# Kernel optimization log

Hardware: AMD Instinct MI355X
Metric: run time of the kernel (lower is better)

Reference implementation:

```python
import jax, jax.numpy as jnp
import numpy as np

H, HP, NH_M, NH_D = 1024, 64, 8, 8
B, T = 2, 2048
SPARSITY = 8
N_ROT = 32  # int(0.5 * HP), even
BASE = 10000.0


def _rope(x, pos, n_rot, base):
    # x: (..., L, d); pos: broadcastable to (..., L). Rotates first n_rot dims.
    half = n_rot // 2
    inv = base ** (-jnp.arange(half, dtype=x.dtype) / half)  # (half,)
    ang = pos[..., None] * inv                               # (..., L, half)
    cos, sin = jnp.cos(ang), jnp.sin(ang)
    x1, x2 = x[..., :half], x[..., half:n_rot]
    rot = jnp.concatenate([x1 * cos - x2 * sin, x1 * sin + x2 * cos], axis=-1)
    return jnp.concatenate([rot, x[..., n_rot:]], axis=-1)


def setup_inputs() -> dict:
    key = jax.random.key(0)
    ks = jax.random.split(key, 6)
    s = 0.02
    return {
        "X": jax.random.normal(ks[0], (B, T, H), jnp.float32),
        "mosa_router_w": jax.random.normal(ks[1], (H, NH_M), jnp.float32) * s,
        "mosa_wqkv": jax.random.normal(ks[2], (H, NH_M, 3 * HP), jnp.float32) * s,
        "mosa_wo": jax.random.normal(ks[3], (NH_M * HP, H), jnp.float32) * s,
        "dense_wqkv": jax.random.normal(ks[4], (H, NH_D, 3 * HP), jnp.float32) * s,
        "dense_wo": jax.random.normal(ks[5], (NH_D * HP, H), jnp.float32) * s,
    }


def _mosa_branch(X, router_w, wqkv, wo):
    # Expert-choice sparse attention: each head routes its own top-k tokens.
    b, t, _ = X.shape
    k = t // SPARSITY
    scores = jnp.einsum('bth,hn->bnt', X, router_w)                      # (b,nh,T)
    _, idx = jax.lax.top_k(scores, k)                                    # (b,nh,k)
    idx = jnp.sort(idx, axis=-1)                                         # keep temporal order
    gates = jax.nn.sigmoid(jnp.take_along_axis(scores, idx, axis=-1))    # (b,nh,k)
    Xg = jnp.take_along_axis(X[:, None], idx[..., None], axis=2)         # (b,nh,k,h)
    qkv = jnp.einsum('bnkh,hnd->bnkd', Xg, wqkv)                         # (b,nh,k,3hp)
    Q, K, V = jnp.split(qkv, 3, axis=-1)
    pos = idx.astype(X.dtype)                                            # original positions for RoPE
    Q = _rope(Q, pos, N_ROT, BASE)
    K = _rope(K, pos, N_ROT, BASE)
    att = jnp.einsum('bnqd,bnkd->bnqk', Q, K) / jnp.sqrt(jnp.asarray(HP, X.dtype))
    causal = idx[..., :, None] >= idx[..., None, :]                      # causality by original index
    att = jnp.where(causal, att, -jnp.inf)
    AV = jnp.einsum('bnqk,bnkd->bnqd', jax.nn.softmax(att, axis=-1), V)
    AV = AV * gates[..., None]
    # scatter selected-token outputs back to full sequence
    out = jnp.zeros((b, NH_M, t, HP), X.dtype)
    bi = jnp.arange(b)[:, None, None]
    hi = jnp.arange(NH_M)[None, :, None]
    out = out.at[bi, hi, idx].set(AV)                                    # (b,nh,T,hp)
    out = out.transpose(0, 2, 1, 3).reshape(b, t, NH_M * HP)
    return out @ wo


def _dense_branch(X, wqkv, wo):
    b, t, _ = X.shape
    qkv = jnp.einsum('bth,hnd->bntd', X, wqkv)                           # (b,nh,T,3hp)
    Q, K, V = jnp.split(qkv, 3, axis=-1)
    pos = jnp.arange(t, dtype=X.dtype)
    Q = _rope(Q, pos, N_ROT, BASE)
    K = _rope(K, pos, N_ROT, BASE)
    att = jnp.einsum('bnqd,bnkd->bnqk', Q, K) / jnp.sqrt(jnp.asarray(HP, X.dtype))
    causal = jnp.tril(jnp.ones((t, t), bool))
    att = jnp.where(causal, att, -jnp.inf)
    AV = jnp.einsum('bnqk,bnkd->bnqd', jax.nn.softmax(att, axis=-1), V)  # (b,nh,T,hp)
    return AV.transpose(0, 2, 1, 3).reshape(b, t, NH_D * HP) @ wo


def reference(X, mosa_router_w, mosa_wqkv, mosa_wo, dense_wqkv, dense_wo):
    return (_mosa_branch(X, mosa_router_w, mosa_wqkv, mosa_wo)
            + _dense_branch(X, dense_wqkv, dense_wo))
```

## Files before the change

kernel.cpp:

```cpp
#include <hip/hip_runtime.h>
#include <math.h>

constexpr int BB = 2;
constexpr int SEQ = 2048;
constexpr int HD = 1024;
constexpr int DH = 64;
constexpr int NHEAD = 8;
constexpr int D3 = 192;
constexpr int KSEL = 256;
constexpr float NEG = -1e30f;

typedef short short8 __attribute__((ext_vector_type(8)));
typedef float f32x4 __attribute__((ext_vector_type(4)));

__device__ __forceinline__ ushort bf16u(float f) {
  union { float f; unsigned u; } v; v.f = f;
  unsigned r = (v.u + 0x7FFFu + ((v.u >> 16) & 1u)) >> 16;
  return (ushort)r;
}
__device__ __forceinline__ float bf2f(ushort h) {
  union { unsigned u; float f; } v; v.u = ((unsigned)h) << 16;
  return v.f;
}

__device__ __forceinline__ unsigned long long rankkey(float s, int idx) {
  union { float f; unsigned u; } v; v.f = s;
  unsigned o = (v.u & 0x80000000u) ? ~v.u : (v.u | 0x80000000u);
  return ((unsigned long long)o << 11) | (unsigned)(2047 - idx);
}

__global__ void cast_bf16x4(const float* __restrict__ x, ushort* __restrict__ y, int n4) {
  int i = blockIdx.x * 256 + threadIdx.x;
  if (i >= n4) return;
  float4 v = ((const float4*)x)[i];
  ushort4 r; r.x = bf16u(v.x); r.y = bf16u(v.y); r.z = bf16u(v.z); r.w = bf16u(v.w);
  ((ushort4*)y)[i] = r;
}

__global__ __launch_bounds__(256) void transpose_cast2(
    const float* __restrict__ W1, ushort* __restrict__ T1,
    const float* __restrict__ W2, ushort* __restrict__ T2, int K, int N) {
  const float* W = blockIdx.z ? W2 : W1;
  ushort* Wt = blockIdx.z ? T2 : T1;
  __shared__ float tile[32][33];
  int n0 = blockIdx.x * 32, k0 = blockIdx.y * 32;
  int tx = threadIdx.x & 31, ty = threadIdx.x >> 5;
#pragma unroll
  for (int i = 0; i < 4; i++)
    tile[ty + 8 * i][tx] = W[(size_t)(k0 + ty + 8 * i) * N + n0 + tx];
  __syncthreads();
#pragma unroll
  for (int i = 0; i < 4; i++)
    Wt[(size_t)(n0 + ty + 8 * i) * K + k0 + tx] = bf16u(tile[tx][ty + 8 * i]);
}

__global__ __launch_bounds__(256) void router2(const float* __restrict__ X,
    const float* __restrict__ rw, float* __restrict__ scores) {
  __shared__ float rwT[8][8][132];
  int tid = threadIdx.x;
  for (int idx = tid; idx < 8192; idx += 256) {
    int h = idx & 1023, n = idx >> 10;
    rwT[n][h >> 7][h & 127] = rw[h * 8 + n];
  }
  __syncthreads();
  int row = blockIdx.x * 32 + (tid >> 3);
  int seg = tid & 7;
  const float* xrow = X + (size_t)row * HD + seg * 128;
  float acc[8] = {};
#pragma unroll 8
  for (int it = 0; it < 32; it++) {
    float4 xv = *(const float4*)(xrow + 4 * it);
#pragma unroll
    for (int n = 0; n < 8; n++) {
      float4 rv = *(const float4*)&rwT[n][seg][4 * it];
      acc[n] += xv.x * rv.x + xv.y * rv.y + xv.z * rv.z + xv.w * rv.w;
    }
  }
#pragma unroll
  for (int n = 0; n < 8; n++) {
    acc[n] += __shfl_xor(acc[n], 1);
    acc[n] += __shfl_xor(acc[n], 2);
    acc[n] += __shfl_xor(acc[n], 4);
  }
  int b = row >> 11, t2 = row & (SEQ - 1);
  scores[((size_t)b * NHEAD + seg) * SEQ + t2] = acc[seg];
}

__global__ __launch_bounds__(256) void topk_partial(const float* __restrict__ scores,
    int* __restrict__ pranks) {
  int row = blockIdx.x;
  int c = blockIdx.y;
  __shared__ unsigned long long ck[64];
  const float* sp = scores + (size_t)row * SEQ;
  int tid = threadIdx.x;
  if (tid < 64) ck[tid] = rankkey(sp[c * 64 + tid], c * 64 + tid);
  __syncthreads();
  unsigned long long kv[8]; int p[8];
#pragma unroll
  for (int i = 0; i < 8; i++) {
    int vi = i * 256 + tid;
    kv[i] = rankkey(sp[vi], vi);
    p[i] = 0;
  }
#pragma unroll 8
  for (int j = 0; j < 64; j += 2) {
    unsigned long long k0 = ck[j], k1 = ck[j + 1];
#pragma unroll
    for (int i = 0; i < 8; i++) {
      p[i] += (k0 > kv[i]);
      p[i] += (k1 > kv[i]);
    }
  }
#pragma unroll
  for (int i = 0; i < 8; i++)
    pranks[((size_t)row * 32 + c) * SEQ + i * 256 + tid] = p[i];
}

__global__ __launch_bounds__(1024) void topk_select(const float* __restrict__ scores,
    const int* __restrict__ pranks, int* __restrict__ sel, float* __restrict__ gates) {
  int bn = blockIdx.x;
  __shared__ int wsum[16];
  int tid = threadIdx.x;
  int t0 = tid * 2;
  int r0 = 0, r1 = 0;
#pragma unroll
  for (int c = 0; c < 32; c++) {
    const int2 pp = *(const int2*)&pranks[((size_t)bn * 32 + c) * SEQ + t0];
    r0 += pp.x; r1 += pp.y;
  }
  int f0 = r0 < KSEL, f1 = r1 < KSEL;
  unsigned long long b0 = __ballot(f0), b1 = __ballot(f1);
  int lane = tid & 63, wv = tid >> 6;
  unsigned long long lower = (1ULL << lane) - 1ULL;
  int before = __popcll(b0 & lower) + __popcll(b1 & lower);
  int wtotal = __popcll(b0) + __popcll(b1);
  if (lane == 0) wsum[wv] = wtotal;
  __syncthreads();
  int woff = 0;
#pragma unroll
  for (int i2 = 0; i2 < 16; i2++) woff += (i2 < wv) ? wsum[i2] : 0;
  int base = woff + before;
  if (f0) { sel[bn * KSEL + base] = t0;
            gates[bn * KSEL + base] = 1.f / (1.f + __expf(-scores[(size_t)bn * SEQ + t0]));
            base++; }
  if (f1) { sel[bn * KSEL + base] = t0 + 1;
            gates[bn * KSEL + base] = 1.f / (1.f + __expf(-scores[(size_t)bn * SEQ + t0 + 1])); }
}

__global__ __launch_bounds__(256) void gemm_mosa_bf16(const ushort* __restrict__ Xb,
    const ushort* __restrict__ Wt, const int* __restrict__ sel,
    ushort* __restrict__ Qmg, ushort* __restrict__ Kmg, ushort* __restrict__ Vtmg) {
  __shared__ __align__(16) ushort As[64][40];
  __shared__ __align__(16) ushort Bs[64][40];
  int bn = blockIdx.x; int b = bn >> 3, n = bn & 7;
  int m0 = blockIdx.y * 64, n0 = blockIdx.z * 64;
  int tid = threadIdx.x;
  int lane = tid & 63, w = tid >> 6;
  int wm = w & 1, wn = w >> 1;
  int cc = lane & 15, quad = lane >> 4;
  int sr = tid >> 2, sc4 = tid & 3;

  int grow = sel[bn * KSEL + m0 + sr];
  const ushort* arow = Xb + ((size_t)(b * SEQ) + grow) * HD;
  const ushort* brow = Wt + ((size_t)(n * D3 + n0 + sr)) * HD;

  f32x4 acc[2][2];
#pragma unroll
  for (int i = 0; i < 2; i++)
#pragma unroll
    for (int j = 0; j < 2; j++)
#pragma unroll
      for (int r = 0; r < 4; r++) acc[i][j][r] = 0.f;

  for (int k0 = 0; k0 < HD; k0 += 32) {
    __syncthreads();
    *(short8*)&As[sr][8 * sc4] = *(const short8*)(arow + k0 + 8 * sc4);
    *(short8*)&Bs[sr][8 * sc4] = *(const short8*)(brow + k0 + 8 * sc4);
    __syncthreads();
    short8 af[2], bf_[2];
#pragma unroll
    for (int i = 0; i < 2; i++) af[i] = *(const short8*)&As[32 * wm + 16 * i + cc][8 * quad];
#pragma unroll
    for (int j = 0; j < 2; j++) bf_[j] = *(const short8*)&Bs[32 * wn + 16 * j + cc][8 * quad];
#pragma unroll
    for (int i = 0; i < 2; i++)
#pragma unroll
      for (int j = 0; j < 2; j++)
        acc[i][j] = __builtin_amdgcn_mfma_f32_16x16x32_bf16(af[i], bf_[j], acc[i][j], 0, 0, 0);
  }

#pragma unroll
  for (int i = 0; i < 2; i++)
#pragma unroll
    for (int j = 0; j < 2; j++) {
      int col = n0 + 32 * wn + 16 * j + cc;
      int row0 = m0 + 32 * wm + 16 * i + 4 * quad;
      if (col < 64) {
#pragma unroll
        for (int r = 0; r < 4; r++)
          Qmg[((size_t)bn * KSEL + row0 + r) * 64 + col] = bf16u(acc[i][j][r] * 0.125f);
      } else if (col < 128) {
#pragma unroll
        for (int r = 0; r < 4; r++)
          Kmg[((size_t)bn * KSEL + row0 + r) * 64 + (col - 64)] = bf16u(acc[i][j][r]);
      } else {
        ushort4 pk;
        pk.x = bf16u(acc[i][j][0]); pk.y = bf16u(acc[i][j][1]);
        pk.z = bf16u(acc[i][j][2]); pk.w = bf16u(acc[i][j][3]);
        *(ushort4*)&Vtmg[((size_t)bn * 64 + (col - 128)) * KSEL + row0] = pk;
      }
    }
}

__global__ void rope_split(ushort* __restrict__ Qb, ushort* __restrict__ Kb,
                           const int* __restrict__ sel, int mosa) {
  int tid = blockIdx.x * 256 + threadIdx.x;
  int j = tid & 15;
  int which = (tid >> 4) & 1;
  int row = tid >> 5;
  float pos = mosa ? (float)sel[row] : (float)(row & (SEQ - 1));
  float inv = __expf((float)j * -0.5756462732485115f);
  float ang = pos * inv;
  float c = cosf(ang), sn = sinf(ang);
  ushort* p = (which ? Kb : Qb) + (size_t)row * 64 + j;
  float x1 = bf2f(p[0]), x2 = bf2f(p[16]);
  p[0] = bf16u(x1 * c - x2 * sn);
  p[16] = bf16u(x1 * sn + x2 * c);
}

template <bool MOSA>
__global__ __launch_bounds__(512) void flash4(
    const ushort* __restrict__ Qg, const ushort* __restrict__ Kg,
    const ushort* __restrict__ Vtg, const int* __restrict__ sel,
    const float* __restrict__ gates, ushort* __restrict__ outp, int nqt) {
  __shared__ __align__(16) ushort Qs[2][64][64];
  __shared__ __align__(16) ushort Ks[64][64];
  __shared__ __align__(16) ushort Vt[64][64];
  __shared__ __align__(16) ushort Ps[2][64][64];

  const int T = MOSA ? KSEL : SEQ;
  int bn = blockIdx.y; int b = bn >> 3, n = bn & 7;
  int pair = blockIdx.x;
  int qtA = pair, qtB = nqt - 1 - pair;
  int tid = threadIdx.x;
  int g = tid >> 8;
  int myqt = g ? qtB : qtA;
  int t = tid & 255;
  int lane = tid & 63, w = (tid >> 6) & 3;
  int cc = lane & 15, quad = lane >> 4;

  const ushort* Qb = Qg + (size_t)bn * T * 64;
  const ushort* Kb = Kg + (size_t)bn * T * 64;
  const ushort* Vb = Vtg + (size_t)bn * 64 * T;

  {
    int r = t >> 2, c = t & 3;
    const ushort* src = Qb + (size_t)(myqt * 64 + r) * 64;
    *(short8*)&Qs[g][r][8 * (c ^ (r & 7))] = *(const short8*)(src + 8 * c);
    int c2 = c + 4;
    *(short8*)&Qs[g][r][8 * (c2 ^ (r & 7))] = *(const short8*)(src + 8 * c2);
  }

  f32x4 oacc[4];
  float m = NEG, l = 0.f;
#pragma unroll
  for (int jd = 0; jd < 4; jd++)
#pragma unroll
    for (int r = 0; r < 4; r++) oacc[jd][r] = 0.f;

  for (int kt = 0; kt <= qtB; kt++) {
    __syncthreads();
    {
      int r = tid >> 3, c = tid & 7;
      *(short8*)&Ks[r][8 * (c ^ (r & 7))] =
          *(const short8*)(Kb + (size_t)(kt * 64 + r) * 64 + 8 * c);
      *(short8*)&Vt[r][8 * (c ^ (r & 7))] =
          *(const short8*)(Vb + (size_t)r * T + kt * 64 + 8 * c);
    }
    __syncthreads();

    if (g || (kt <= qtA)) {
      f32x4 sacc[4];
#pragma unroll
      for (int j = 0; j < 4; j++)
#pragma unroll
        for (int r = 0; r < 4; r++) sacc[j][r] = 0.f;
      int qrow = 16 * w + cc;
#pragma unroll
      for (int ks = 0; ks < 2; ks++) {
        short8 bq = *(const short8*)&Qs[g][qrow][8 * ((quad + 4 * ks) ^ (qrow & 7))];
#pragma unroll
        for (int j = 0; j < 4; j++) {
          int krow = 16 * j + cc;
          short8 ak = *(const short8*)&Ks[krow][8 * ((quad + 4 * ks) ^ (krow & 7))];
          sacc[j] = __builtin_amdgcn_mfma_f32_16x16x32_bf16(ak, bq, sacc[j], 0, 0, 0);
        }
      }
      if (kt == myqt) {
#pragma unroll
        for (int j = 0; j < 4; j++)
#pragma unroll
          for (int r = 0; r < 4; r++)
            if (16 * j + 4 * quad + r > 16 * w + cc) sacc[j][r] = NEG;
      }
      float mx = NEG;
#pragma unroll
      for (int j = 0; j < 4; j++)
#pragma unroll
        for (int r = 0; r < 4; r++) mx = fmaxf(mx, sacc[j][r]);
      mx = fmaxf(mx, __shfl_xor(mx, 16));
      mx = fmaxf(mx, __shfl_xor(mx, 32));
      float mn = fmaxf(m, mx);
      float sc = __expf(m - mn);
      m = mn;
      float rsum = 0.f;
      float p[4][4];
#pragma unroll
      for (int j = 0; j < 4; j++)
#pragma unroll
        for (int r = 0; r < 4; r++) { p[j][r] = __expf(sacc[j][r] - mn); rsum += p[j][r]; }
      rsum += __shfl_xor(rsum, 16);
      rsum += __shfl_xor(rsum, 32);
      l = l * sc + rsum;
#pragma unroll
      for (int j = 0; j < 4; j++) {
        ushort4 pk;
        pk.x = bf16u(p[j][0]); pk.y = bf16u(p[j][1]);
        pk.z = bf16u(p[j][2]); pk.w = bf16u(p[j][3]);
        int phys = (2 * j + (quad >> 1)) ^ (qrow & 7);
        *(ushort4*)&Ps[g][qrow][phys * 8 + 4 * (quad & 1)] = pk;
      }
#pragma unroll
      for (int r = 0; r < 4; r++) {
        float scr = __shfl(sc, 16 * quad + 4 * quad + r);
#pragma unroll
        for (int jd = 0; jd < 4; jd++) oacc[jd][r] *= scr;
      }
      __asm__ volatile("s_waitcnt lgkmcnt(0)" ::: "memory");
#pragma unroll
      for (int ks = 0; ks < 2; ks++) {
        short8 ap = *(const short8*)&Ps[g][qrow][8 * ((quad + 4 * ks) ^ (qrow & 7))];
#pragma unroll
        for (int jd = 0; jd < 4; jd++) {
          int vrow = 16 * jd + cc;
          short8 bv = *(const short8*)&Vt[vrow][8 * ((quad + 4 * ks) ^ (vrow & 7))];
          oacc[jd] = __builtin_amdgcn_mfma_f32_16x16x32_bf16(ap, bv, oacc[jd], 0, 0, 0);
        }
      }
    }
  }

#pragma unroll
  for (int r = 0; r < 4; r++) {
    float lr = __shfl(l, 16 * quad + 4 * quad + r);
    int q = myqt * 64 + 16 * w + 4 * quad + r;
    float scale;
    size_t row;
    if (MOSA) {
      int trow = sel[bn * KSEL + q];
      scale = gates[bn * KSEL + q] / lr;
      row = (size_t)(b * SEQ + trow);
    } else {
      scale = 1.f / lr;
      row = (size_t)(b * SEQ + q);
    }
    ushort* orow = outp + row * (NHEAD * DH) + n * DH;
#pragma unroll
    for (int jd = 0; jd < 4; jd++)
      orow[16 * jd + cc] = bf16u(oacc[jd][r] * scale);
  }
}

template <int MODE>
__global__ __launch_bounds__(256) void gemm_bf16(
    const ushort* __restrict__ A1, const ushort* __restrict__ B1t, int K1,
    const ushort* __restrict__ A2, const ushort* __restrict__ B2t, int K2,
    void* __restrict__ outv, int N,
    ushort* __restrict__ Qo, ushort* __restrict__ Ko, ushort* __restrict__ Vto) {
  __shared__ __align__(16) ushort As[128][32];
  __shared__ __align__(16) ushort Bs[128][32];
  int m0 = blockIdx.x * 128, n0 = blockIdx.y * 128;
  int tid = threadIdx.x;
  int lane = tid & 63, wave = tid >> 6;
  int wm = wave & 1, wn = wave >> 1;
  int cc = lane & 15, quad = lane >> 4;
  int sr = tid >> 2, sc = tid & 3;

  f32x4 acc[4][4];
#pragma unroll
  for (int i = 0; i < 4; i++)
#pragma unroll
    for (int j = 0; j < 4; j++)
#pragma unroll
      for (int r = 0; r < 4; r++) acc[i][j][r] = 0.f;

  const int npass = (MODE == 0) ? 2 : 1;
  for (int pass = 0; pass < npass; pass++) {
    const ushort* A = pass ? A2 : A1;
    const ushort* Bt = pass ? B2t : B1t;
    int K = pass ? K2 : K1;
    for (int k0 = 0; k0 < K; k0 += 32) {
      __syncthreads();
      {
        short8 a0 = *(const short8*)(A + (size_t)(m0 + sr) * K + k0 + 8 * sc);
        short8 a1 = *(const short8*)(A + (size_t)(m0 + sr + 64) * K + k0 + 8 * sc);
        short8 b0 = *(const short8*)(Bt + (size_t)(n0 + sr) * K + k0 + 8 * sc);
        short8 b1 = *(const short8*)(Bt + (size_t)(n0 + sr + 64) * K + k0 + 8 * sc);
        *(short8*)&As[sr][8 * ((sc + (sr >> 1)) & 3)] = a0;
        *(short8*)&As[sr + 64][8 * ((sc + ((sr + 64) >> 1)) & 3)] = a1;
        *(short8*)&Bs[sr][8 * ((sc + (sr >> 1)) & 3)] = b0;
        *(short8*)&Bs[sr + 64][8 * ((sc + ((sr + 64) >> 1)) & 3)] = b1;
      }
      __syncthreads();
      short8 af[4], bfr[4];
#pragma unroll
      for (int i = 0; i < 4; i++) {
        int ra = 64 * wm + 16 * i + cc;
        af[i] = *(const short8*)&As[ra][8 * ((quad + (ra >> 1)) & 3)];
      }
#pragma unroll
      for (int j = 0; j < 4; j++) {
        int rb = 64 * wn + 16 * j + cc;
        bfr[j] = *(const short8*)&Bs[rb][8 * ((quad + (rb >> 1)) & 3)];
      }
#pragma unroll
      for (int i = 0; i < 4; i++)
#pragma unroll
        for (int j = 0; j < 4; j++)
          acc[i][j] = __builtin_amdgcn_mfma_f32_16x16x32_bf16(af[i], bfr[j], acc[i][j], 0, 0, 0);
    }
  }

#pragma unroll
  for (int i = 0; i < 4; i++) {
#pragma unroll
    for (int j = 0; j < 4; j++) {
      int colg = n0 + 64 * wn + 16 * j + cc;
      int row0 = m0 + 64 * wm + 16 * i + 4 * quad;
      if (MODE == 0) {
#pragma unroll
        for (int r = 0; r < 4; r++)
          ((float*)outv)[(size_t)(row0 + r) * N + colg] = acc[i][j][r];
      } else {
        int nn = colg / 192, c = colg % 192;
        int b2 = row0 >> 11, t2 = row0 & 2047;
        int bn2 = b2 * 8 + nn;
        if (c < 64) {
#pragma unroll
          for (int r = 0; r < 4; r++)
            Qo[((size_t)bn2 * SEQ + t2 + r) * 64 + c] = bf16u(acc[i][j][r] * 0.125f);
        } else if (c < 128) {
#pragma unroll
          for (int r = 0; r < 4; r++)
            Ko[((size_t)bn2 * SEQ + t2 + r) * 64 + (c - 64)] = bf16u(acc[i][j][r]);
        } else {
          ushort4 pk;
          pk.x = bf16u(acc[i][j][0]); pk.y = bf16u(acc[i][j][1]);
          pk.z = bf16u(acc[i][j][2]); pk.w = bf16u(acc[i][j][3]);
          *(ushort4*)&Vto[((size_t)bn2 * 64 + (c - 128)) * SEQ + t2] = pk;
        }
      }
    }
  }
}

extern "C" void kernel_launch(void* const* d_in, const int* in_sizes, int n_in,
                              void* d_out, int out_size, void* d_ws, size_t ws_size,
                              hipStream_t stream) {
  const float* X          = (const float*)d_in[0];
  const float* router_w   = (const float*)d_in[1];
  const float* mosa_wqkv  = (const float*)d_in[2];
  const float* mosa_wo    = (const float*)d_in[3];
  const float* dense_wqkv = (const float*)d_in[4];
  const float* dense_wo   = (const float*)d_in[5];
  float* out = (float*)d_out;
  char* ws = (char*)d_ws;

  float*  scores  = (float*) (ws + 0);
  int*    sel     = (int*)   (ws + 131072);
  float*  gates   = (float*) (ws + 147456);
  ushort* avm     = (ushort*)(ws + 163840);
  ushort* avd     = (ushort*)(ws + 4358144);
  ushort* Xb      = (ushort*)(ws + 8552448);
  ushort* Wqkv_t  = (ushort*)(ws + 16941056);
  ushort* Wmq_t   = (ushort*)(ws + 20086784);
  ushort* Wdo_t   = (ushort*)(ws + 23232512);
  ushort* Wmo_t   = (ushort*)(ws + 24281088);
  ushort* Qg      = (ushort*)(ws + 25329664);
  ushort* Kg      = (ushort*)(ws + 29523968);
  ushort* Vtg     = (ushort*)(ws + 33718272);
  ushort* Qmg     = (ushort*)(ws + 37912576);
  ushort* Kmg     = (ushort*)(ws + 38436864);
  ushort* Vtmg    = (ushort*)(ws + 38961152);
  int*    pranks  = (int*)   (ws + 39485440);

  hipMemsetAsync(avm, 0, (size_t)BB * SEQ * NHEAD * DH * sizeof(ushort), stream);

  cast_bf16x4<<<4096, 256, 0, stream>>>(X, Xb, BB * SEQ * HD / 4);
  transpose_cast2<<<dim3(48, 32, 2), 256, 0, stream>>>(dense_wqkv, Wqkv_t,
                                                       mosa_wqkv, Wmq_t, 1024, 1536);
  transpose_cast2<<<dim3(32, 16, 2), 256, 0, stream>>>(dense_wo, Wdo_t,
                                                       mosa_wo, Wmo_t, 512, 1024);

  router2<<<BB * SEQ / 32, 256, 0, stream>>>(X, router_w, scores);
  topk_partial<<<dim3(BB * NHEAD, 32), 256, 0, stream>>>(scores, pranks);
  topk_select<<<BB * NHEAD, 1024, 0, stream>>>(scores, pranks, sel, gates);

  gemm_mosa_bf16<<<dim3(BB * NHEAD, KSEL / 64, D3 / 64), 256, 0, stream>>>(
      Xb, Wmq_t, sel, Qmg, Kmg, Vtmg);
  rope_split<<<(BB * NHEAD * KSEL * 32) / 256, 256, 0, stream>>>(Qmg, Kmg, sel, 1);
  flash4<true><<<dim3((KSEL / 64) / 2, BB * NHEAD), 512, 0, stream>>>(
      Qmg, Kmg, Vtmg, sel, gates, avm, KSEL / 64);

  gemm_bf16<1><<<dim3(32, 12), 256, 0, stream>>>(Xb, Wqkv_t, 1024,
      (const ushort*)nullptr, (const ushort*)nullptr, 0, nullptr, NHEAD * D3,
      Qg, Kg, Vtg);
  rope_split<<<(BB * NHEAD * SEQ * 32) / 256, 256, 0, stream>>>(Qg, Kg, nullptr, 0);
  flash4<false><<<dim3((SEQ / 64) / 2, BB * NHEAD), 512, 0, stream>>>(
      Qg, Kg, Vtg, (const int*)nullptr, (const float*)nullptr, avd, SEQ / 64);

  gemm_bf16<0><<<dim3(32, 8), 256, 0, stream>>>(avm, Wmo_t, 512, avd, Wdo_t, 512, out, HD,
                                                nullptr, nullptr, nullptr);
}
```

Measured before the change: 246.7 us.

## Merge dense and MoSA flash attention into one launch with async double-buffered KV

Replaces the two templated flash4 launches, which used paired query tiles per 512-thread block, with a single flash5 launch. Each 256-thread block handles one query tile, and the blocks are ordered longest-first across both the dense and MoSA branches. K/V tiles are double-buffered in LDS using global_load_lds direct-to-LDS copies, so the next tile's fetch overlaps compute, and Q stays in registers. The goal is to cut launch overhead, hide load latency and improve load balancing. The cost is the loss of the causal-pair balancing inside each block, plus reliance on the LDS swizzle being reproduced through the per-lane source addressing.

Measured after the change: 238.8 us. -3.2%, faster.

```diff
diff --git a/kernel.cpp b/kernel.cpp
--- a/kernel.cpp
+++ b/kernel.cpp
@@ -21,6 +21,12 @@
 __device__ __forceinline__ float bf2f(ushort h) {
   union { unsigned u; float f; } v; v.u = ((unsigned)h) << 16;
   return v.f;
+}
+
+__device__ __forceinline__ void gl_lds16(const ushort* g, ushort* l) {
+  __builtin_amdgcn_global_load_lds(
+      (const __attribute__((address_space(1))) unsigned int*)g,
+      (__attribute__((address_space(3))) unsigned int*)l, 16, 0, 0);
 }
 
 __device__ __forceinline__ unsigned long long rankkey(float s, int idx) {
@@ -228,38 +234,56 @@
   p[16] = bf16u(x1 * sn + x2 * c);
 }
 
-template <bool MOSA>
-__global__ __launch_bounds__(512) void flash4(
+__global__ __launch_bounds__(256) void flash5(
     const ushort* __restrict__ Qg, const ushort* __restrict__ Kg,
-    const ushort* __restrict__ Vtg, const int* __restrict__ sel,
-    const float* __restrict__ gates, ushort* __restrict__ outp, int nqt) {
-  __shared__ __align__(16) ushort Qs[2][64][64];
-  __shared__ __align__(16) ushort Ks[64][64];
-  __shared__ __align__(16) ushort Vt[64][64];
-  __shared__ __align__(16) ushort Ps[2][64][64];
-
-  const int T = MOSA ? KSEL : SEQ;
-  int bn = blockIdx.y; int b = bn >> 3, n = bn & 7;
-  int pair = blockIdx.x;
-  int qtA = pair, qtB = nqt - 1 - pair;
+    const ushort* __restrict__ Vtg,
+    const ushort* __restrict__ Qmg, const ushort* __restrict__ Kmg,
+    const ushort* __restrict__ Vtmg,
+    const int* __restrict__ sel, const float* __restrict__ gates,
+    ushort* __restrict__ avd, ushort* __restrict__ avm) {
+  __shared__ __align__(16) ushort Ks[2][64][64];
+  __shared__ __align__(16) ushort Vt[2][64][64];
+  __shared__ __align__(16) ushort Ps[64][64];
+
+  int bx = blockIdx.x;
+  bool mosa = bx >= 512;
+  int bn, qt, T;
+  const ushort *Qb, *Kb, *Vb;
+  ushort* outp;
+  if (!mosa) {
+    bn = bx & 15; qt = 31 - (bx >> 4); T = SEQ;
+    Qb = Qg + (size_t)bn * SEQ * 64;
+    Kb = Kg + (size_t)bn * SEQ * 64;
+    Vb = Vtg + (size_t)bn * 64 * SEQ;
+    outp = avd;
+  } else {
+    int rr = bx - 512;
+    bn = rr & 15; qt = 3 - (rr >> 4); T = KSEL;
+    Qb = Qmg + (size_t)bn * KSEL * 64;
+    Kb = Kmg + (size_t)bn * KSEL * 64;
+    Vb = Vtmg + (size_t)bn * 64 * KSEL;
+    outp = avm;
+  }
+  int b = bn >> 3, n = bn & 7;
   int tid = threadIdx.x;
-  int g = tid >> 8;
-  int myqt = g ? qtB : qtA;
-  int t = tid & 255;
-  int lane = tid & 63, w = (tid >> 6) & 3;
+  int lane = tid & 63, w = tid >> 6;
   int cc = lane & 15, quad = lane >> 4;
-
-  const ushort* Qb = Qg + (size_t)bn * T * 64;
-  const ushort* Kb = Kg + (size_t)bn * T * 64;
-  const ushort* Vb = Vtg + (size_t)bn * 64 * T;
-
+  int qrow = 16 * w + cc;
+
+  short8 bq[2];
   {
-    int r = t >> 2, c = t & 3;
-    const ushort* src = Qb + (size_t)(myqt * 64 + r) * 64;
-    *(short8*)&Qs[g][r][8 * (c ^ (r & 7))] = *(const short8*)(src + 8 * c);
-    int c2 = c + 4;
-    *(short8*)&Qs[g][r][8 * (c2 ^ (r & 7))] = *(const short8*)(src + 8 * c2);
-  }
+    const ushort* qsrc = Qb + (size_t)(qt * 64 + qrow) * 64;
+    bq[0] = *(const short8*)(qsrc + 8 * quad);
+    bq[1] = *(const short8*)(qsrc + 8 * (quad + 4));
+  }
+
+  int rloc = lane >> 3;
+  int c_log = (lane & 7) ^ rloc;
+  int row0 = 16 * w + rloc, row1 = row0 + 8;
+  const ushort* pK0 = Kb + (size_t)row0 * 64 + 8 * c_log;
+  const ushort* pK1 = Kb + (size_t)row1 * 64 + 8 * c_log;
+  const ushort* pV0 = Vb + (size_t)row0 * T + 8 * c_log;
+  const ushort* pV1 = Vb + (size_t)row1 * T + 8 * c_log;
 
   f32x4 oacc[4];
   float m = NEG, l = 0.f;
@@ -268,84 +292,85 @@
 #pragma unroll
     for (int r = 0; r < 4; r++) oacc[jd][r] = 0.f;
 
-  for (int kt = 0; kt <= qtB; kt++) {
+  gl_lds16(pK0, &Ks[0][16 * w][0]);
+  gl_lds16(pK1, &Ks[0][16 * w + 8][0]);
+  gl_lds16(pV0, &Vt[0][16 * w][0]);
+  gl_lds16(pV1, &Vt[0][16 * w + 8][0]);
+
+  for (int kt = 0; kt <= qt; kt++) {
+    int buf = kt & 1;
     __syncthreads();
-    {
-      int r = tid >> 3, c = tid & 7;
-      *(short8*)&Ks[r][8 * (c ^ (r & 7))] =
-          *(const short8*)(Kb + (size_t)(kt * 64 + r) * 64 + 8 * c);
-      *(short8*)&Vt[r][8 * (c ^ (r & 7))] =
-          *(const short8*)(Vb + (size_t)r * T + kt * 64 + 8 * c);
-    }
-    __syncthreads();
-
-    if (g || (kt <= qtA)) {
-      f32x4 sacc[4];
+    if (kt < qt) {
+      int nk = kt + 1, nb = buf ^ 1;
+      gl_lds16(pK0 + (size_t)nk * 4096, &Ks[nb][16 * w][0]);
+      gl_lds16(pK1 + (size_t)nk * 4096, &Ks[nb][16 * w + 8][0]);
+      gl_lds16(pV0 + nk * 64, &Vt[nb][16 * w][0]);
+      gl_lds16(pV1 + nk * 64, &Vt[nb][16 * w + 8][0]);
+    }
+
+    f32x4 sacc[4];
+#pragma unroll
+    for (int j = 0; j < 4; j++)
+#pragma unroll
+      for (int r = 0; r < 4; r++) sacc[j][r] = 0.f;
+#pragma unroll
+    for (int ks = 0; ks < 2; ks++) {
+#pragma unroll
+      for (int j = 0; j < 4; j++) {
+        int krow = 16 * j + cc;
+        short8 ak = *(const short8*)&Ks[buf][krow][8 * ((quad + 4 * ks) ^ (krow & 7))];
+        sacc[j] = __builtin_amdgcn_mfma_f32_16x16x32_bf16(ak, bq[ks], sacc[j], 0, 0, 0);
+      }
+    }
+    if (kt == qt) {
 #pragma unroll
       for (int j = 0; j < 4; j++)
 #pragma unroll
-        for (int r = 0; r < 4; r++) sacc[j][r] = 0.f;
-      int qrow = 16 * w + cc;
-#pragma unroll
-      for (int ks = 0; ks < 2; ks++) {
-        short8 bq = *(const short8*)&Qs[g][qrow][8 * ((quad + 4 * ks) ^ (qrow & 7))];
-#pragma unroll
-        for (int j = 0; j < 4; j++) {
-          int krow = 16 * j + cc;
-          short8 ak = *(const short8*)&Ks[krow][8 * ((quad + 4 * ks) ^ (krow & 7))];
-          sacc[j] = __builtin_amdgcn_mfma_f32_16x16x32_bf16(ak, bq, sacc[j], 0, 0, 0);
-        }
-      }
-      if (kt == myqt) {
-#pragma unroll
-        for (int j = 0; j < 4; j++)
-#pragma unroll
-          for (int r = 0; r < 4; r++)
-            if (16 * j + 4 * quad + r > 16 * w + cc) sacc[j][r] = NEG;
-      }
-      float mx = NEG;
-#pragma unroll
-      for (int j = 0; j < 4; j++)
-#pragma unroll
-        for (int r = 0; r < 4; r++) mx = fmaxf(mx, sacc[j][r]);
-      mx = fmaxf(mx, __shfl_xor(mx, 16));
-      mx = fmaxf(mx, __shfl_xor(mx, 32));
-      float mn = fmaxf(m, mx);
-      float sc = __expf(m - mn);
-      m = mn;
-      float rsum = 0.f;
-      float p[4][4];
-#pragma unroll
-      for (int j = 0; j < 4; j++)
-#pragma unroll
-        for (int r = 0; r < 4; r++) { p[j][r] = __expf(sacc[j][r] - mn); rsum += p[j][r]; }
-      rsum += __shfl_xor(rsum, 16);
-      rsum += __shfl_xor(rsum, 32);
-      l = l * sc + rsum;
-#pragma unroll
-      for (int j = 0; j < 4; j++) {
-        ushort4 pk;
-        pk.x = bf16u(p[j][0]); pk.y = bf16u(p[j][1]);
-        pk.z = bf16u(p[j][2]); pk.w = bf16u(p[j][3]);
-        int phys = (2 * j + (quad >> 1)) ^ (qrow & 7);
-        *(ushort4*)&Ps[g][qrow][phys * 8 + 4 * (quad & 1)] = pk;
-      }
-#pragma unroll
-      for (int r = 0; r < 4; r++) {
-        float scr = __shfl(sc, 16 * quad + 4 * quad + r);
-#pragma unroll
-        for (int jd = 0; jd < 4; jd++) oacc[jd][r] *= scr;
-      }
-      __asm__ volatile("s_waitcnt lgkmcnt(0)" ::: "memory");
-#pragma unroll
-      for (int ks = 0; ks < 2; ks++) {
-        short8 ap = *(const short8*)&Ps[g][qrow][8 * ((quad + 4 * ks) ^ (qrow & 7))];
-#pragma unroll
-        for (int jd = 0; jd < 4; jd++) {
-          int vrow = 16 * jd + cc;
-          short8 bv = *(const short8*)&Vt[vrow][8 * ((quad + 4 * ks) ^ (vrow & 7))];
-          oacc[jd] = __builtin_amdgcn_mfma_f32_16x16x32_bf16(ap, bv, oacc[jd], 0, 0, 0);
-        }
+        for (int r = 0; r < 4; r++)
+          if (16 * j + 4 * quad + r > qrow) sacc[j][r] = NEG;
+    }
+    float mx = NEG;
+#pragma unroll
+    for (int j = 0; j < 4; j++)
+#pragma unroll
+      for (int r = 0; r < 4; r++) mx = fmaxf(mx, sacc[j][r]);
+    mx = fmaxf(mx, __shfl_xor(mx, 16));
+    mx = fmaxf(mx, __shfl_xor(mx, 32));
+    float mn = fmaxf(m, mx);
+    float sc = __expf(m - mn);
+    m = mn;
+    float rsum = 0.f;
+    float p[4][4];
+#pragma unroll
+    for (int j = 0; j < 4; j++)
+#pragma unroll
+      for (int r = 0; r < 4; r++) { p[j][r] = __expf(sacc[j][r] - mn); rsum += p[j][r]; }
+    rsum += __shfl_xor(rsum, 16);
+    rsum += __shfl_xor(rsum, 32);
+    l = l * sc + rsum;
+#pragma unroll
+    for (int j = 0; j < 4; j++) {
+      ushort4 pk;
+      pk.x = bf16u(p[j][0]); pk.y = bf16u(p[j][1]);
+      pk.z = bf16u(p[j][2]); pk.w = bf16u(p[j][3]);
+      int phys = (2 * j + (quad >> 1)) ^ (qrow & 7);
+      *(ushort4*)&Ps[qrow][phys * 8 + 4 * (quad & 1)] = pk;
+    }
+#pragma unroll
+    for (int r = 0; r < 4; r++) {
+      float scr = __shfl(sc, 16 * quad + 4 * quad + r);
+#pragma unroll
+      for (int jd = 0; jd < 4; jd++) oacc[jd][r] *= scr;
+    }
+    __asm__ volatile("s_waitcnt lgkmcnt(0)" ::: "memory");
+#pragma unroll
+    for (int ks = 0; ks < 2; ks++) {
+      short8 ap = *(const short8*)&Ps[qrow][8 * ((quad + 4 * ks) ^ (qrow & 7))];
+#pragma unroll
+      for (int jd = 0; jd < 4; jd++) {
+        int vrow = 16 * jd + cc;
+        short8 bv = *(const short8*)&Vt[buf][vrow][8 * ((quad + 4 * ks) ^ (vrow & 7))];
+        oacc[jd] = __builtin_amdgcn_mfma_f32_16x16x32_bf16(ap, bv, oacc[jd], 0, 0, 0);
       }
     }
   }
@@ -353,10 +378,10 @@
 #pragma unroll
   for (int r = 0; r < 4; r++) {
     float lr = __shfl(l, 16 * quad + 4 * quad + r);
-    int q = myqt * 64 + 16 * w + 4 * quad + r;
+    int q = qt * 64 + 16 * w + 4 * quad + r;
     float scale;
     size_t row;
-    if (MOSA) {
+    if (mosa) {
       int trow = sel[bn * KSEL + q];
       scale = gates[bn * KSEL + q] / lr;
       row = (size_t)(b * SEQ + trow);
@@ -509,15 +534,12 @@
   gemm_mosa_bf16<<<dim3(BB * NHEAD, KSEL / 64, D3 / 64), 256, 0, stream>>>(
       Xb, Wmq_t, sel, Qmg, Kmg, Vtmg);
   rope_split<<<(BB * NHEAD * KSEL * 32) / 256, 256, 0, stream>>>(Qmg, Kmg, sel, 1);
-  flash4<true><<<dim3((KSEL / 64) / 2, BB * NHEAD), 512, 0, stream>>>(
-      Qmg, Kmg, Vtmg, sel, gates, avm, KSEL / 64);
-
   gemm_bf16<1><<<dim3(32, 12), 256, 0, stream>>>(Xb, Wqkv_t, 1024,
       (const ushort*)nullptr, (const ushort*)nullptr, 0, nullptr, NHEAD * D3,
       Qg, Kg, Vtg);
   rope_split<<<(BB * NHEAD * SEQ * 32) / 256, 256, 0, stream>>>(Qg, Kg, nullptr, 0);
-  flash4<false><<<dim3((SEQ / 64) / 2, BB * NHEAD), 512, 0, stream>>>(
-      Qg, Kg, Vtg, (const int*)nullptr, (const float*)nullptr, avd, SEQ / 64);
+
+  flash5<<<576, 256, 0, stream>>>(Qg, Kg, Vtg, Qmg, Kmg, Vtmg, sel, gates, avd, avm);
 
   gemm_bf16<0><<<dim3(32, 8), 256, 0, stream>>>(avm, Wmo_t, 512, avd, Wdo_t, 512, out, HD,
                                                 nullptr, nullptr, nullptr);
```
